# Performance work log

Measured on AMD Instinct MI355X. Metric: run time of the kernel, lower is better.

Reference implementation:

```python
import jax, jax.numpy as jnp
import numpy as np

B, S, D = 8, 1024, 768
H = 12
HD = D // H  # 64
SCALE = 1.0 / (HD ** 0.5)


def setup_inputs() -> dict:
    key = jax.random.key(0)
    ks = jax.random.split(key, 5)
    x = jax.random.normal(ks[0], (B, S, D), dtype=jnp.float32)
    W_qkv = jax.random.normal(ks[1], (D, 3 * D), dtype=jnp.float32) * 0.02
    b_qkv = jax.random.normal(ks[2], (3 * D,), dtype=jnp.float32) * 0.02
    W_proj = jax.random.normal(ks[3], (D, D), dtype=jnp.float32) * 0.02
    b_proj = jax.random.normal(ks[4], (D,), dtype=jnp.float32) * 0.02
    return {"x": x, "W_qkv": W_qkv, "b_qkv": b_qkv, "W_proj": W_proj, "b_proj": b_proj}


def reference(x, W_qkv, b_qkv, W_proj, b_proj):
    b, s, d = x.shape
    # QKV projection: (B, S, 3D) -> (3, B, H, S, HD)
    qkv = x @ W_qkv + b_qkv
    qkv = qkv.reshape(b, s, 3, H, HD).transpose(2, 0, 3, 1, 4)
    q, k, v = qkv[0], qkv[1], qkv[2]
    # scaled dot-product attention (full matrix, as in the original)
    scores = jnp.einsum("bhqd,bhkd->bhqk", q, k) * SCALE
    attn = jax.nn.softmax(scores, axis=-1)
    out = jnp.einsum("bhqk,bhkd->bhqd", attn, v)
    # merge heads: (B, S, D)
    out = out.transpose(0, 2, 1, 3).reshape(b, s, d)
    return out @ W_proj + b_proj
```

## Files before the change

kernel.cpp:

```cpp
#include <hip/hip_runtime.h>
#include <math.h>

typedef __attribute__((ext_vector_type(8))) unsigned short ushortx8;
typedef __attribute__((ext_vector_type(8))) __bf16 bf16x8;
typedef __attribute__((ext_vector_type(4))) float floatx4;
typedef __attribute__((ext_vector_type(16))) float floatx16;

#define NH 12
#define SEQ 1024
#define DM 768
#define HD 64
#define GK 768
#define QK_SCALE 0.18033688011112042f

#define GLDS16(gp, lp) __builtin_amdgcn_global_load_lds( \
    (const __attribute__((address_space(1))) unsigned int*)(const void*)(gp), \
    (__attribute__((address_space(3))) unsigned int*)(lp), 16, 0, 0)

__device__ __forceinline__ unsigned short f2bf(float f) {
    union { float f; unsigned u; } v; v.f = f;
    unsigned r = v.u + 0x7fffu + ((v.u >> 16) & 1u);
    return (unsigned short)(r >> 16);
}

__device__ __forceinline__ unsigned pk2bf(float f0, float f1) {
    union { float f; unsigned u; } a, b; a.f = f0; b.f = f1;
    return ((a.u + 0x8000u) >> 16) | ((b.u + 0x8000u) & 0xffff0000u);
}

__device__ __forceinline__ float fast_exp2(float x) {
    float r;
    asm("v_exp_f32 %0, %1" : "=v"(r) : "v"(x));
    return r;
}

__global__ void k_prep(const float* __restrict__ x, unsigned short* __restrict__ x_bf,
                       const float* __restrict__ Wqkv, unsigned short* __restrict__ WqkvT,
                       const float* __restrict__ Wproj, unsigned short* __restrict__ WprojT) {
    __shared__ float tile[32][33];
    int bx = blockIdx.x;
    if (bx < 6144) {
        int i = bx * 256 + threadIdx.x;
        float4 v = ((const float4*)x)[i];
        ushort4 o;
        o.x = f2bf(v.x); o.y = f2bf(v.y); o.z = f2bf(v.z); o.w = f2bf(v.w);
        ((ushort4*)x_bf)[i] = o;
        return;
    }
    const float* in; unsigned short* out; int R, C, c0, r0;
    if (bx < 7872) {
        int t = bx - 6144;
        in = Wqkv; out = WqkvT; R = 768; C = 2304;
        c0 = (t % 72) * 32; r0 = (t / 72) * 32;
    } else {
        int t = bx - 7872;
        in = Wproj; out = WprojT; R = 768; C = 768;
        c0 = (t % 24) * 32; r0 = (t / 24) * 32;
    }
    int tx = threadIdx.x & 31, ty = threadIdx.x >> 5;
#pragma unroll
    for (int i = 0; i < 4; i++)
        tile[ty + 8 * i][tx] = in[(size_t)(r0 + ty + 8 * i) * C + c0 + tx];
    __syncthreads();
#pragma unroll
    for (int i = 0; i < 4; i++)
        out[(size_t)(c0 + ty + 8 * i) * R + r0 + tx] = f2bf(tile[tx][ty + 8 * i]);
}

__device__ __forceinline__ void stage6(const unsigned short* gA, const unsigned short* gB,
                                       unsigned short* lbuf, int w, int k0) {
#pragma unroll
    for (int g = 0; g < 4; g++)
        GLDS16(gA + (size_t)(w * 64 + g * 16) * GK + k0, lbuf + (w * 64 + g * 16) * 32);
#pragma unroll
    for (int g = 0; g < 2; g++)
        GLDS16(gB + (size_t)(w * 32 + g * 16) * GK + k0, lbuf + 8192 + (w * 32 + g * 16) * 32);
}

__device__ __forceinline__ void mfma24(const unsigned short* Ab, const unsigned short* Bb,
                                       int wm, int wn, int l15, int csw,
                                       floatx4 (&acc)[8][3]) {
    bf16x8 af[8], bfr[3];
#pragma unroll
    for (int m = 0; m < 8; m++)
        af[m] = __builtin_bit_cast(bf16x8,
            *(const ushortx8*)&Ab[(wm * 128 + m * 16 + l15) * 32 + csw]);
#pragma unroll
    for (int n = 0; n < 3; n++)
        bfr[n] = __builtin_bit_cast(bf16x8,
            *(const ushortx8*)&Bb[(wn * 48 + n * 16 + l15) * 32 + csw]);
#pragma unroll
    for (int m = 0; m < 8; m++)
#pragma unroll
        for (int n = 0; n < 3; n++)
            acc[m][n] = __builtin_amdgcn_mfma_f32_16x16x32_bf16(af[m], bfr[n], acc[m][n], 0, 0, 0);
}

__device__ __forceinline__ void gemm_mainloop(const unsigned short* __restrict__ A,
                                              const unsigned short* __restrict__ Bt,
                                              unsigned short* smem, int m0, int n0,
                                              int w, int lane, floatx4 (&acc)[8][3]) {
    int quad = lane >> 4, l15 = lane & 15;
    int wm = w >> 1, wn = w & 1;
    int rA = lane >> 2;
    int cSwz = ((lane & 3) ^ ((lane >> 3) & 3)) * 8;
    int csw = (quad ^ ((l15 >> 1) & 3)) * 8;
    const unsigned short* gA = A + (size_t)(m0 + rA) * GK + cSwz;
    const unsigned short* gB = Bt + (size_t)(n0 + rA) * GK + cSwz;

    stage6(gA, gB, smem, w, 0);
    stage6(gA, gB, smem + 12288, w, 32);
#pragma unroll 1
    for (int t = 0; t < 24; t++) {
        if (t < 23) asm volatile("s_waitcnt vmcnt(6)" ::: "memory");
        else        asm volatile("s_waitcnt vmcnt(0)" ::: "memory");
        __builtin_amdgcn_s_barrier();
        asm volatile("" ::: "memory");
        const unsigned short* Ab = smem + (t & 1) * 12288;
        __builtin_amdgcn_s_setprio(1);
        mfma24(Ab, Ab + 8192, wm, wn, l15, csw, acc);
        __builtin_amdgcn_s_setprio(0);
        asm volatile("" ::: "memory");
        __builtin_amdgcn_s_barrier();
        asm volatile("" ::: "memory");
        if (t < 22) stage6(gA, gB, smem + (t & 1) * 12288, w, (t + 2) * 32);
    }
}

__global__ __launch_bounds__(256, 3) void k_gemm_qkv(
    const unsigned short* __restrict__ A, const unsigned short* __restrict__ Bt,
    const float* __restrict__ bias,
    unsigned short* __restrict__ Qb, unsigned short* __restrict__ Kb,
    unsigned short* __restrict__ Vt) {
    __shared__ unsigned short smem[25344];
    int tid = threadIdx.x;
    int w = tid >> 6, lane = tid & 63;
    int quad = lane >> 4, l15 = lane & 15;
    int wm = w >> 1, wn = w & 1;
    int lin = blockIdx.x;
    int xcd = lin & 7, slot = lin >> 3;
    int mt_i = xcd * 4 + (slot & 3);
    int nt_i = slot >> 2;
    int m0 = mt_i * 256, n0 = nt_i * 96;

    floatx4 acc[8][3] = {};
    gemm_mainloop(A, Bt, smem, m0, n0, w, lane, acc);

    int tsel = nt_i / 8;
    int bb = m0 >> 10;
    int s_base0 = (m0 & 1023) + wm * 128;
    if (tsel < 2) {
        unsigned short* __restrict__ dst = (tsel == 0) ? Qb : Kb;
#pragma unroll
        for (int m = 0; m < 8; m++) {
            int s_base = s_base0 + m * 16 + quad * 4;
#pragma unroll
            for (int n = 0; n < 3; n++) {
                int n_g = n0 + wn * 48 + n * 16 + l15;
                int nloc = n_g - tsel * 768;
                int hh = nloc >> 6, dd = nloc & 63;
                float bv = bias[n_g];
                size_t base = ((size_t)(bb * NH + hh) * SEQ + s_base) * HD + dd;
                if (tsel == 0) {
#pragma unroll
                    for (int rg = 0; rg < 4; rg++)
                        dst[base + (size_t)rg * HD] = f2bf((acc[m][n][rg] + bv) * QK_SCALE);
                } else {
#pragma unroll
                    for (int rg = 0; rg < 4; rg++)
                        dst[base + (size_t)rg * HD] = f2bf(acc[m][n][rg] + bv);
                }
            }
        }
    } else {
        __syncthreads();
#pragma unroll
        for (int m = 0; m < 8; m++) {
#pragma unroll
            for (int n = 0; n < 3; n++) {
                int col = wn * 48 + n * 16 + l15;
                float bv = bias[n0 + col];
                ushort4 pk;
                pk.x = f2bf(acc[m][n][0] + bv);
                pk.y = f2bf(acc[m][n][1] + bv);
                pk.z = f2bf(acc[m][n][2] + bv);
                pk.w = f2bf(acc[m][n][3] + bv);
                *(ushort4*)&smem[col * 264 + wm * 128 + m * 16 + quad * 4] = pk;
            }
        }
        __syncthreads();
        if (tid < 192) {
            int col = tid >> 1, part = tid & 1;
            int dglob = (n0 - 1536) + col;
            int hh = dglob >> 6, dd = dglob & 63;
            size_t gbase = ((size_t)(bb * NH + hh) * HD + dd) * SEQ + (m0 & 1023) + part * 128;
#pragma unroll
            for (int i = 0; i < 16; i++)
                *(uint4*)&Vt[gbase + i * 8] = *(const uint4*)&smem[col * 264 + part * 128 + i * 8];
        }
    }
}

__global__ __launch_bounds__(256) void k_attn(
    const unsigned short* __restrict__ Qb, const unsigned short* __restrict__ Kb,
    const unsigned short* __restrict__ Vt, unsigned short* __restrict__ attn_out) {
    __shared__ unsigned short Ks[64 * 64];
    __shared__ unsigned short Vts[64 * 64];
    __shared__ unsigned short Pt[4][32 * 72];
    int tid = threadIdx.x;
    int w = tid >> 6, lane = tid & 63;
    int l31 = lane & 31, lh = lane >> 5;
    int lin = blockIdx.x;
    int xcd = lin & 7, slot = lin >> 3;
    int bh = xcd * 12 + (slot >> 3);
    int qt = slot & 7;
    int b = bh / NH, h = bh - b * NH;
    const unsigned short* Qp = Qb + (size_t)bh * SEQ * HD;
    const unsigned short* Kp = Kb + (size_t)bh * SEQ * HD;
    const unsigned short* Vp = Vt + (size_t)bh * HD * SEQ;
    int q0w = qt * 128 + w * 32;
    unsigned short* Ptw = &Pt[w][0];

    bf16x8 qf[4];
#pragma unroll
    for (int ds = 0; ds < 4; ds++)
        qf[ds] = __builtin_bit_cast(bf16x8,
            *(const ushortx8*)&Qp[(size_t)(q0w + l31) * HD + ds * 16 + lh * 8]);

    floatx16 o[2] = {};
    float lsum = 0.f;

    int rr = tid >> 3, cc8 = (tid & 7) * 8;
    int cs = cc8 ^ ((rr & 7) * 8);
    int rsw = (l31 & 7) * 8;
    uint4 kr0 = *(const uint4*)&Kp[(size_t)rr * HD + cc8];
    uint4 kr1 = *(const uint4*)&Kp[(size_t)(rr + 32) * HD + cc8];
    uint4 vr0 = *(const uint4*)&Vp[(size_t)rr * SEQ + cc8];
    uint4 vr1 = *(const uint4*)&Vp[(size_t)(rr + 32) * SEQ + cc8];

    for (int kb = 0; kb < SEQ; kb += 64) {
        __syncthreads();
        *(uint4*)&Ks[rr * 64 + cs] = kr0;
        *(uint4*)&Ks[(rr + 32) * 64 + cs] = kr1;
        *(uint4*)&Vts[rr * 64 + cs] = vr0;
        *(uint4*)&Vts[(rr + 32) * 64 + cs] = vr1;
        if (kb + 64 < SEQ) {
            kr0 = *(const uint4*)&Kp[(size_t)(kb + 64 + rr) * HD + cc8];
            kr1 = *(const uint4*)&Kp[(size_t)(kb + 64 + rr + 32) * HD + cc8];
            vr0 = *(const uint4*)&Vp[(size_t)rr * SEQ + kb + 64 + cc8];
            vr1 = *(const uint4*)&Vp[(size_t)(rr + 32) * SEQ + kb + 64 + cc8];
        }
        __syncthreads();

        floatx16 sc[2] = {};
        __builtin_amdgcn_s_setprio(1);
#pragma unroll
        for (int mt = 0; mt < 2; mt++)
#pragma unroll
            for (int ds = 0; ds < 4; ds++) {
                bf16x8 kf = __builtin_bit_cast(bf16x8,
                    *(const ushortx8*)&Ks[(mt * 32 + l31) * 64 + ((ds * 16 + lh * 8) ^ rsw)]);
                sc[mt] = __builtin_amdgcn_mfma_f32_32x32x16_bf16(kf, qf[ds], sc[mt], 0, 0, 0);
            }
        __builtin_amdgcn_s_setprio(0);

        float p0[16], p1[16];
#pragma unroll
        for (int r = 0; r < 16; r++) {
            p0[r] = fast_exp2(sc[0][r]);
            p1[r] = fast_exp2(sc[1][r]);
            lsum += p0[r] + p1[r];
        }

        uint4 pw[4];
#pragma unroll
        for (int mt = 0; mt < 2; mt++) {
            const float* pp = mt ? p1 : p0;
#pragma unroll
            for (int hf = 0; hf < 2; hf++) {
                unsigned a, bq, c, d;
                asm("v_cvt_pk_bf16_f32 %0, %1, %2" : "=v"(a)  : "v"(pp[hf * 8 + 0]), "v"(pp[hf * 8 + 1]));
                asm("v_cvt_pk_bf16_f32 %0, %1, %2" : "=v"(bq) : "v"(pp[hf * 8 + 4]), "v"(pp[hf * 8 + 5]));
                asm("v_cvt_pk_bf16_f32 %0, %1, %2" : "=v"(c)  : "v"(pp[hf * 8 + 2]), "v"(pp[hf * 8 + 3]));
                asm("v_cvt_pk_bf16_f32 %0, %1, %2" : "=v"(d)  : "v"(pp[hf * 8 + 6]), "v"(pp[hf * 8 + 7]));
                asm("v_permlane32_swap_b32 %0, %1" : "+v"(a), "+v"(bq));
                asm("v_permlane32_swap_b32 %0, %1" : "+v"(c), "+v"(d));
                uint4 wv; wv.x = a; wv.y = c; wv.z = bq; wv.w = d;
                pw[mt * 2 + hf] = wv;
            }
        }

        __builtin_amdgcn_s_setprio(1);
#pragma unroll
        for (int ks = 0; ks < 4; ks++) {
            bf16x8 pf = __builtin_bit_cast(bf16x8, pw[ks]);
#pragma unroll
            for (int mt = 0; mt < 2; mt++) {
                bf16x8 vf = __builtin_bit_cast(bf16x8,
                    *(const ushortx8*)&Vts[(mt * 32 + l31) * 64 + ((ks * 16 + lh * 8) ^ rsw)]);
                o[mt] = __builtin_amdgcn_mfma_f32_32x32x16_bf16(vf, pf, o[mt], 0, 0, 0);
            }
        }
        __builtin_amdgcn_s_setprio(0);
    }

    lsum += __shfl_xor(lsum, 32, 64);
    float inv = 1.0f / lsum;

#pragma unroll
    for (int mt = 0; mt < 2; mt++)
#pragma unroll
        for (int g = 0; g < 4; g++) {
            uint2 pk;
            pk.x = pk2bf(o[mt][g * 4 + 0] * inv, o[mt][g * 4 + 1] * inv);
            pk.y = pk2bf(o[mt][g * 4 + 2] * inv, o[mt][g * 4 + 3] * inv);
            *(uint2*)&Ptw[l31 * 72 + mt * 32 + g * 8 + lh * 4] = pk;
        }
    __builtin_amdgcn_s_barrier();
#pragma unroll
    for (int pass = 0; pass < 4; pass++) {
        int row = pass * 8 + (lane >> 3);
        int col8 = (lane & 7) * 8;
        uint4 vv = *(const uint4*)&Ptw[row * 72 + col8];
        *(uint4*)&attn_out[(size_t)(b * SEQ + q0w + row) * DM + h * HD + col8] = vv;
    }
}

__global__ __launch_bounds__(256, 3) void k_gemm_proj(
    const unsigned short* __restrict__ A, const unsigned short* __restrict__ Bt,
    const float* __restrict__ bias, float* __restrict__ out) {
    __shared__ unsigned short smem[24576];
    int tid = threadIdx.x;
    int w = tid >> 6, lane = tid & 63;
    int quad = lane >> 4, l15 = lane & 15;
    int wm = w >> 1, wn = w & 1;
    int lin = blockIdx.x;
    int xcd = lin & 7, slot = lin >> 3;
    int mt_i = xcd * 4 + (slot & 3);
    int nt_i = slot >> 2;
    int m0 = mt_i * 256, n0 = nt_i * 96;

    floatx4 acc[8][3] = {};
    gemm_mainloop(A, Bt, smem, m0, n0, w, lane, acc);

#pragma unroll
    for (int m = 0; m < 8; m++) {
        int m_base = m0 + wm * 128 + m * 16 + quad * 4;
#pragma unroll
        for (int n = 0; n < 3; n++) {
            int n_g = n0 + wn * 48 + n * 16 + l15;
            float bv = bias[n_g];
#pragma unroll
            for (int rg = 0; rg < 4; rg++)
                out[(size_t)(m_base + rg) * DM + n_g] = acc[m][n][rg] + bv;
        }
    }
}

extern "C" void kernel_launch(void* const* d_in, const int* in_sizes, int n_in,
                              void* d_out, int out_size, void* d_ws, size_t ws_size,
                              hipStream_t stream) {
    const float* x     = (const float*)d_in[0];
    const float* Wqkv  = (const float*)d_in[1];
    const float* bqkv  = (const float*)d_in[2];
    const float* Wproj = (const float*)d_in[3];
    const float* bproj = (const float*)d_in[4];
    float* out = (float*)d_out;

    char* ws = (char*)d_ws;
    unsigned short* x_bf   = (unsigned short*)(ws);
    unsigned short* WqkvT  = (unsigned short*)(ws + 12582912);
    unsigned short* WprojT = (unsigned short*)(ws + 16121856);
    unsigned short* Qb     = (unsigned short*)(ws + 17301504);
    unsigned short* Kb     = (unsigned short*)(ws + 29884416);
    unsigned short* Vt     = (unsigned short*)(ws + 42467328);
    unsigned short* attn   = (unsigned short*)(ws + 55050240);

    k_prep<<<8448, 256, 0, stream>>>(x, x_bf, Wqkv, WqkvT, Wproj, WprojT);
    k_gemm_qkv<<<768, 256, 0, stream>>>(x_bf, WqkvT, bqkv, Qb, Kb, Vt);
    k_attn<<<768, 256, 0, stream>>>(Qb, Kb, Vt, attn);
    k_gemm_proj<<<256, 256, 0, stream>>>(attn, WprojT, bproj, out);
}
```

Baseline: 185.6 us.

## Double-buffer K/V tiles in attention and retile projection GEMM with async LDS loads

```diff
diff --git a/kernel.cpp b/kernel.cpp
--- a/kernel.cpp
+++ b/kernel.cpp
@@ -204,8 +204,8 @@
 __global__ __launch_bounds__(256) void k_attn(
     const unsigned short* __restrict__ Qb, const unsigned short* __restrict__ Kb,
     const unsigned short* __restrict__ Vt, unsigned short* __restrict__ attn_out) {
-    __shared__ unsigned short Ks[64 * 64];
-    __shared__ unsigned short Vts[64 * 64];
+    __shared__ unsigned short Ks[2][64 * 64];
+    __shared__ unsigned short Vts[2][64 * 64];
     __shared__ unsigned short Pt[4][32 * 72];
     int tid = threadIdx.x;
     int w = tid >> 6, lane = tid & 63;
@@ -233,24 +233,37 @@
     int rr = tid >> 3, cc8 = (tid & 7) * 8;
     int cs = cc8 ^ ((rr & 7) * 8);
     int rsw = (l31 & 7) * 8;
-    uint4 kr0 = *(const uint4*)&Kp[(size_t)rr * HD + cc8];
-    uint4 kr1 = *(const uint4*)&Kp[(size_t)(rr + 32) * HD + cc8];
-    uint4 vr0 = *(const uint4*)&Vp[(size_t)rr * SEQ + cc8];
-    uint4 vr1 = *(const uint4*)&Vp[(size_t)(rr + 32) * SEQ + cc8];
+
+    {
+        uint4 a = *(const uint4*)&Kp[(size_t)rr * HD + cc8];
+        uint4 b2 = *(const uint4*)&Kp[(size_t)(rr + 32) * HD + cc8];
+        uint4 c = *(const uint4*)&Vp[(size_t)rr * SEQ + cc8];
+        uint4 d = *(const uint4*)&Vp[(size_t)(rr + 32) * SEQ + cc8];
+        *(uint4*)&Ks[0][rr * 64 + cs] = a;
+        *(uint4*)&Ks[0][(rr + 32) * 64 + cs] = b2;
+        *(uint4*)&Vts[0][rr * 64 + cs] = c;
+        *(uint4*)&Vts[0][(rr + 32) * 64 + cs] = d;
+    }
+    uint4 kr0 = *(const uint4*)&Kp[(size_t)(64 + rr) * HD + cc8];
+    uint4 kr1 = *(const uint4*)&Kp[(size_t)(64 + rr + 32) * HD + cc8];
+    uint4 vr0 = *(const uint4*)&Vp[(size_t)rr * SEQ + 64 + cc8];
+    uint4 vr1 = *(const uint4*)&Vp[(size_t)(rr + 32) * SEQ + 64 + cc8];
+    __syncthreads();
 
     for (int kb = 0; kb < SEQ; kb += 64) {
-        __syncthreads();
-        *(uint4*)&Ks[rr * 64 + cs] = kr0;
-        *(uint4*)&Ks[(rr + 32) * 64 + cs] = kr1;
-        *(uint4*)&Vts[rr * 64 + cs] = vr0;
-        *(uint4*)&Vts[(rr + 32) * 64 + cs] = vr1;
+        int cur = (kb >> 6) & 1;
         if (kb + 64 < SEQ) {
-            kr0 = *(const uint4*)&Kp[(size_t)(kb + 64 + rr) * HD + cc8];
-            kr1 = *(const uint4*)&Kp[(size_t)(kb + 64 + rr + 32) * HD + cc8];
-            vr0 = *(const uint4*)&Vp[(size_t)rr * SEQ + kb + 64 + cc8];
-            vr1 = *(const uint4*)&Vp[(size_t)(rr + 32) * SEQ + kb + 64 + cc8];
-        }
-        __syncthreads();
+            *(uint4*)&Ks[cur ^ 1][rr * 64 + cs] = kr0;
+            *(uint4*)&Ks[cur ^ 1][(rr + 32) * 64 + cs] = kr1;
+            *(uint4*)&Vts[cur ^ 1][rr * 64 + cs] = vr0;
+            *(uint4*)&Vts[cur ^ 1][(rr + 32) * 64 + cs] = vr1;
+            if (kb + 128 < SEQ) {
+                kr0 = *(const uint4*)&Kp[(size_t)(kb + 128 + rr) * HD + cc8];
+                kr1 = *(const uint4*)&Kp[(size_t)(kb + 128 + rr + 32) * HD + cc8];
+                vr0 = *(const uint4*)&Vp[(size_t)rr * SEQ + kb + 128 + cc8];
+                vr1 = *(const uint4*)&Vp[(size_t)(rr + 32) * SEQ + kb + 128 + cc8];
+            }
+        }
 
         floatx16 sc[2] = {};
         __builtin_amdgcn_s_setprio(1);
@@ -259,7 +272,7 @@
 #pragma unroll
             for (int ds = 0; ds < 4; ds++) {
                 bf16x8 kf = __builtin_bit_cast(bf16x8,
-                    *(const ushortx8*)&Ks[(mt * 32 + l31) * 64 + ((ds * 16 + lh * 8) ^ rsw)]);
+                    *(const ushortx8*)&Ks[cur][(mt * 32 + l31) * 64 + ((ds * 16 + lh * 8) ^ rsw)]);
                 sc[mt] = __builtin_amdgcn_mfma_f32_32x32x16_bf16(kf, qf[ds], sc[mt], 0, 0, 0);
             }
         __builtin_amdgcn_s_setprio(0);
@@ -297,11 +310,13 @@
 #pragma unroll
             for (int mt = 0; mt < 2; mt++) {
                 bf16x8 vf = __builtin_bit_cast(bf16x8,
-                    *(const ushortx8*)&Vts[(mt * 32 + l31) * 64 + ((ks * 16 + lh * 8) ^ rsw)]);
+                    *(const ushortx8*)&Vts[cur][(mt * 32 + l31) * 64 + ((ks * 16 + lh * 8) ^ rsw)]);
                 o[mt] = __builtin_amdgcn_mfma_f32_32x32x16_bf16(vf, pf, o[mt], 0, 0, 0);
             }
         }
         __builtin_amdgcn_s_setprio(0);
+
+        __syncthreads();
     }
 
     lsum += __shfl_xor(lsum, 32, 64);
@@ -326,26 +341,77 @@
     }
 }
 
-__global__ __launch_bounds__(256, 3) void k_gemm_proj(
+__device__ __forceinline__ void stage4(const unsigned short* gA, const unsigned short* gB,
+                                       unsigned short* lbuf, int w, int k0) {
+#pragma unroll
+    for (int g = 0; g < 2; g++)
+        GLDS16(gA + (size_t)(w * 32 + g * 16) * GK + k0, lbuf + (w * 32 + g * 16) * 32);
+#pragma unroll
+    for (int g = 0; g < 2; g++)
+        GLDS16(gB + (size_t)(w * 32 + g * 16) * GK + k0, lbuf + 4096 + (w * 32 + g * 16) * 32);
+}
+
+__device__ __forceinline__ void mfma12(const unsigned short* Ab, const unsigned short* Bb,
+                                       int wm, int wn, int l15, int csw,
+                                       floatx4 (&acc)[4][3]) {
+    bf16x8 af[4], bfr[3];
+#pragma unroll
+    for (int m = 0; m < 4; m++)
+        af[m] = __builtin_bit_cast(bf16x8,
+            *(const ushortx8*)&Ab[(wm * 64 + m * 16 + l15) * 32 + csw]);
+#pragma unroll
+    for (int n = 0; n < 3; n++)
+        bfr[n] = __builtin_bit_cast(bf16x8,
+            *(const ushortx8*)&Bb[(wn * 48 + n * 16 + l15) * 32 + csw]);
+#pragma unroll
+    for (int m = 0; m < 4; m++)
+#pragma unroll
+        for (int n = 0; n < 3; n++)
+            acc[m][n] = __builtin_amdgcn_mfma_f32_16x16x32_bf16(af[m], bfr[n], acc[m][n], 0, 0, 0);
+}
+
+__global__ __launch_bounds__(256, 2) void k_gemm_proj(
     const unsigned short* __restrict__ A, const unsigned short* __restrict__ Bt,
     const float* __restrict__ bias, float* __restrict__ out) {
-    __shared__ unsigned short smem[24576];
+    __shared__ unsigned short smem[16384];
     int tid = threadIdx.x;
     int w = tid >> 6, lane = tid & 63;
     int quad = lane >> 4, l15 = lane & 15;
     int wm = w >> 1, wn = w & 1;
     int lin = blockIdx.x;
     int xcd = lin & 7, slot = lin >> 3;
-    int mt_i = xcd * 4 + (slot & 3);
-    int nt_i = slot >> 2;
-    int m0 = mt_i * 256, n0 = nt_i * 96;
-
-    floatx4 acc[8][3] = {};
-    gemm_mainloop(A, Bt, smem, m0, n0, w, lane, acc);
-
-#pragma unroll
-    for (int m = 0; m < 8; m++) {
-        int m_base = m0 + wm * 128 + m * 16 + quad * 4;
+    int mt_i = xcd * 8 + (slot & 7);
+    int nt_i = slot >> 3;
+    int m0 = mt_i * 128, n0 = nt_i * 96;
+
+    int rA = lane >> 2;
+    int cSwz = ((lane & 3) ^ ((lane >> 3) & 3)) * 8;
+    int csw = (quad ^ ((l15 >> 1) & 3)) * 8;
+    const unsigned short* gA = A + (size_t)(m0 + rA) * GK + cSwz;
+    const unsigned short* gB = Bt + (size_t)(n0 + rA) * GK + cSwz;
+
+    floatx4 acc[4][3] = {};
+    stage4(gA, gB, smem, w, 0);
+    stage4(gA, gB, smem + 8192, w, 32);
+#pragma unroll 1
+    for (int t = 0; t < 24; t++) {
+        if (t < 23) asm volatile("s_waitcnt vmcnt(4)" ::: "memory");
+        else        asm volatile("s_waitcnt vmcnt(0)" ::: "memory");
+        __builtin_amdgcn_s_barrier();
+        asm volatile("" ::: "memory");
+        const unsigned short* Ab = smem + (t & 1) * 8192;
+        __builtin_amdgcn_s_setprio(1);
+        mfma12(Ab, Ab + 4096, wm, wn, l15, csw, acc);
+        __builtin_amdgcn_s_setprio(0);
+        asm volatile("" ::: "memory");
+        __builtin_amdgcn_s_barrier();
+        asm volatile("" ::: "memory");
+        if (t < 22) stage4(gA, gB, smem + (t & 1) * 8192, w, (t + 2) * 32);
+    }
+
+#pragma unroll
+    for (int m = 0; m < 4; m++) {
+        int m_base = m0 + wm * 64 + m * 16 + quad * 4;
 #pragma unroll
         for (int n = 0; n < 3; n++) {
             int n_g = n0 + wn * 48 + n * 16 + l15;
@@ -379,5 +445,5 @@
     k_prep<<<8448, 256, 0, stream>>>(x, x_bf, Wqkv, WqkvT, Wproj, WprojT);
     k_gemm_qkv<<<768, 256, 0, stream>>>(x_bf, WqkvT, bqkv, Qb, Kb, Vt);
     k_attn<<<768, 256, 0, stream>>>(Qb, Kb, Vt, attn);
-    k_gemm_proj<<<256, 256, 0, stream>>>(attn, WprojT, bproj, out);
-}
+    k_gemm_proj<<<512, 256, 0, stream>>>(attn, WprojT, bproj, out);
+}
```

Measured after the change: 183.9 us, median of 2. No clear change (-0.9%).
